# Optimization experiments

Hardware: AMD Instinct MI355X
Metric: run time of the kernel (lower is better)

Reference implementation:

```python
import jax, jax.numpy as jnp
import numpy as np

N_NODES = 20000
N_EDGES = 320000
D_IN = 256
DIMS = [512, 256, 128]
NEG_SLOPE = 0.2


def gatv2(x, src, dst, Wl, Wr, att, b, n):
    # GATv2Conv (heads=1, no self loops, no edge_attr)
    xl = x @ Wl                      # [N, D] source transform (lin_l)
    xr = x @ Wr                      # [N, D] target transform (lin_r)
    e = jax.nn.leaky_relu(xl[src] + xr[dst], NEG_SLOPE) @ att  # [E]
    # segment softmax over destination nodes
    m = jax.ops.segment_max(e, dst, num_segments=n)
    ex = jnp.exp(e - m[dst])
    s = jax.ops.segment_sum(ex, dst, num_segments=n)
    alpha = ex / (s[dst] + 1e-16)
    out = jax.ops.segment_sum(alpha[:, None] * xl[src], dst, num_segments=n)
    return out + b


def setup_inputs() -> dict:
    key = jax.random.key(0)
    ks = jax.random.split(key, 32)
    x = jax.random.normal(ks[0], (N_NODES, D_IN), dtype=jnp.float32)
    edge_index = jax.random.randint(ks[1], (2, N_EDGES), 0, N_NODES, dtype=jnp.int32)
    inp = {"x": x, "edge_index": edge_index}
    d_in = D_IN
    ki = 2
    for li, d_out in enumerate(DIMS, start=1):
        sc = 1.0 / np.sqrt(d_in)
        inp[f"Wl{li}"] = jax.random.normal(ks[ki + 0], (d_in, d_out), dtype=jnp.float32) * sc
        inp[f"Wr{li}"] = jax.random.normal(ks[ki + 1], (d_in, d_out), dtype=jnp.float32) * sc
        inp[f"att{li}"] = jax.random.normal(ks[ki + 2], (d_out,), dtype=jnp.float32) * (1.0 / np.sqrt(d_out))
        inp[f"bc{li}"] = jnp.zeros((d_out,), dtype=jnp.float32)
        inp[f"Ws{li}"] = jax.random.normal(ks[ki + 3], (d_in, d_out), dtype=jnp.float32) * sc
        inp[f"bs{li}"] = jnp.zeros((d_out,), dtype=jnp.float32)
        ki += 4
        d_in = d_out
    return inp


def reference(x, edge_index,
              Wl1, Wr1, att1, bc1, Ws1, bs1,
              Wl2, Wr2, att2, bc2, Ws2, bs2,
              Wl3, Wr3, att3, bc3, Ws3, bs3):
    src, dst = edge_index[0], edge_index[1]
    n = x.shape[0]
    h = gatv2(x, src, dst, Wl1, Wr1, att1, bc1, n) + (x @ Ws1 + bs1)
    h = jax.nn.relu(h)
    h = gatv2(h, src, dst, Wl2, Wr2, att2, bc2, n) + (h @ Ws2 + bs2)
    h = jax.nn.relu(h)
    h = gatv2(h, src, dst, Wl3, Wr3, att3, bc3, n) + (h @ Ws3 + bs3)
    return h
```

## Files before the change

kernel.cpp:

```cpp
#include <hip/hip_runtime.h>
#include <hip/hip_bf16.h>
#include <math.h>

#define N_NODES 20000
#define N_EDGES 320000
#define MAXDEG 64

typedef _Float16 f16x8 __attribute__((ext_vector_type(8)));
typedef _Float16 h2 __attribute__((ext_vector_type(2)));
typedef float f32x4 __attribute__((ext_vector_type(4)));

__device__ __forceinline__ unsigned short f2h_bits(float f) {
    _Float16 h = (_Float16)f;
    return __builtin_bit_cast(unsigned short, h);
}

typedef const unsigned int __attribute__((address_space(1)))* gas_ptr;
typedef unsigned int __attribute__((address_space(3)))* las_ptr;
__device__ __forceinline__ void gld16(const unsigned short* g, unsigned short* l) {
    __builtin_amdgcn_global_load_lds((gas_ptr)(const void*)g, (las_ptr)(void*)l, 16, 0, 0);
}

__global__ void scatter_kernel(const int* __restrict__ src, const int* __restrict__ dst,
                               int* __restrict__ cnt, int* __restrict__ csr_pad, int E) {
    int i = blockIdx.x * blockDim.x + threadIdx.x;
    if (i < E) {
        int d = dst[i];
        int pos = atomicAdd(&cnt[d], 1);
        if (pos < MAXDEG) csr_pad[(d << 6) + pos] = src[i];
    }
}

struct PrepJobs {
    const float* W[9];
    unsigned short* Wt[9];
    int K[9];
    int D[9];
    int tbeg[10];
    const float* x;
    unsigned short* xh;
    int nconv4;
    int nconvb;
    int* cnt;
};
__global__ __launch_bounds__(256) void prep_kernel(PrepJobs jb) {
    int bid = blockIdx.x;
    int ntile = jb.tbeg[9];
    if (bid < ntile) {
        __shared__ float ld[32][33];
        int job = 0;
        while (bid >= jb.tbeg[job + 1]) ++job;
        int tl = bid - jb.tbeg[job];
        int K = jb.K[job], D = jb.D[job];
        int TK = K >> 5;
        int td = tl / TK, tk = tl - td * TK;
        int k0 = tk << 5, d0 = td << 5;
        int t = threadIdx.x;
        int c = t & 31, r0 = (t >> 5) << 2;
        const float* Wp = jb.W[job];
#pragma unroll
        for (int jj = 0; jj < 4; ++jj)
            ld[r0 + jj][c] = Wp[(size_t)(k0 + r0 + jj) * D + d0 + c];
        __syncthreads();
        unsigned short* Wtp = jb.Wt[job];
#pragma unroll
        for (int jj = 0; jj < 4; ++jj) {
            int dr = r0 + jj;
            Wtp[(size_t)(d0 + dr) * K + k0 + c] = f2h_bits(ld[c][dr]);
        }
    } else if (bid < ntile + jb.nconvb) {
        int cidx = (bid - ntile) * 256 + (int)threadIdx.x;
        if (cidx < jb.nconv4) {
            int base = cidx * 4;
            float4 v = *(const float4*)(jb.x + base);
            uint2 pk;
            pk.x = (unsigned int)f2h_bits(v.x) | ((unsigned int)f2h_bits(v.y) << 16);
            pk.y = (unsigned int)f2h_bits(v.z) | ((unsigned int)f2h_bits(v.w) << 16);
            *(uint2*)(jb.xh + base) = pk;
        }
    } else {
        int i = (bid - ntile - jb.nconvb) * 256 + (int)threadIdx.x;
        if (i < N_NODES) jb.cnt[i] = 0;
    }
}

template <int SEED_F32>
__global__ __launch_bounds__(256) void gemm3_kernel(
        const unsigned short* __restrict__ A,
        const unsigned short* __restrict__ Bt,
        unsigned short* __restrict__ xlh,
        unsigned short* __restrict__ xrh,
        unsigned short* __restrict__ seedh,
        float* __restrict__ seedf,
        const float* __restrict__ b1,
        const float* __restrict__ b2,
        int M, int K, int D) {
    __shared__ __align__(16) unsigned short Asl[128 * 64];
    __shared__ __align__(16) unsigned short Bsl[128 * 64];

    int NC = (3 * D) >> 7;
    int MT = (M + 127) >> 7;
    int g = blockIdx.x;
    int xcd = g & 7, slot = g >> 3;
    int m_local = slot / NC, c = slot - m_local * NC;
    int mt = m_local * 8 + xcd;
    if (mt >= MT) return;

    int tid = threadIdx.x;
    int wave = tid >> 6, lane = tid & 63;
    int q = lane >> 4, t = lane & 15;
    int wm = (wave & 1) * 64, wn = (wave >> 1) * 64;
    int bm = mt << 7;
    int bn_all = c << 7;
    int seg = bn_all / D;
    int bn = bn_all - seg * D;

    f32x4 acc[4][4];
#pragma unroll
    for (int i = 0; i < 4; ++i)
#pragma unroll
        for (int j = 0; j < 4; ++j) acc[i][j] = (f32x4){0.f, 0.f, 0.f, 0.f};

    for (int k0 = 0; k0 < K; k0 += 64) {
#pragma unroll
        for (int rnd = 0; rnd < 4; ++rnd) {
            int ch = rnd * 256 + tid;
            int row = ch >> 3, part = ch & 7;
            int gr = bm + row; if (gr >= M) gr = M - 1;
            gld16(A + (size_t)gr * K + k0 + part * 8,
                  Asl + (rnd * 256 + wave * 64) * 8);
        }
#pragma unroll
        for (int rnd = 0; rnd < 4; ++rnd) {
            int ch = rnd * 256 + tid;
            int row = ch >> 3, part = ch & 7;
            gld16(Bt + (size_t)(bn_all + row) * K + k0 + part * 8,
                  Bsl + (rnd * 256 + wave * 64) * 8);
        }
        __syncthreads();

#pragma unroll
        for (int kk = 0; kk < 2; ++kk) {
            f16x8 an[4], am[4];
#pragma unroll
            for (int jn = 0; jn < 4; ++jn)
                an[jn] = *(const f16x8*)(Bsl + (wn + jn * 16 + t) * 64 + kk * 32 + q * 8);
#pragma unroll
            for (int im = 0; im < 4; ++im)
                am[im] = *(const f16x8*)(Asl + (wm + im * 16 + t) * 64 + kk * 32 + q * 8);
#pragma unroll
            for (int jn = 0; jn < 4; ++jn)
#pragma unroll
                for (int im = 0; im < 4; ++im)
                    acc[jn][im] = __builtin_amdgcn_mfma_f32_16x16x32_f16(an[jn], am[im], acc[jn][im], 0, 0, 0);
        }
        __syncthreads();
    }

#pragma unroll
    for (int jn = 0; jn < 4; ++jn) {
        int n0 = bn + wn + jn * 16 + q * 4;
        float bx = 0.f, by = 0.f, bz = 0.f, bw = 0.f;
        if (seg == 2) {
            float4 bb1 = *(const float4*)(b1 + n0);
            float4 bb2 = *(const float4*)(b2 + n0);
            bx = bb1.x + bb2.x; by = bb1.y + bb2.y;
            bz = bb1.z + bb2.z; bw = bb1.w + bb2.w;
        }
#pragma unroll
        for (int im = 0; im < 4; ++im) {
            int m = bm + wm + im * 16 + t;
            if (m < M) {
                float v0 = acc[jn][im][0] + bx;
                float v1 = acc[jn][im][1] + by;
                float v2 = acc[jn][im][2] + bz;
                float v3 = acc[jn][im][3] + bw;
                size_t idx = (size_t)m * D + n0;
                if (seg == 2 && SEED_F32) {
                    *(float4*)(seedf + idx) = make_float4(v0, v1, v2, v3);
                } else {
                    uint2 pk;
                    pk.x = (unsigned int)f2h_bits(v0) | ((unsigned int)f2h_bits(v1) << 16);
                    pk.y = (unsigned int)f2h_bits(v2) | ((unsigned int)f2h_bits(v3) << 16);
                    unsigned short* dstp = (seg == 0) ? xlh : (seg == 1) ? xrh : seedh;
                    *(uint2*)(dstp + idx) = pk;
                }
            }
        }
    }
}

template <int D, int SEED_H, int WRITE_H, int RELU>
__global__ __launch_bounds__(128) void fused_agg_kernel(
        const unsigned short* __restrict__ xl,
        const unsigned short* __restrict__ xr,
        const float* __restrict__ att,
        const int* __restrict__ cnt,
        const int* __restrict__ csr_pad,
        const unsigned short* __restrict__ seedh,
        const float* __restrict__ seedf,
        float* __restrict__ outf,
        unsigned short* __restrict__ outh) {
    constexpr int VPL = D / 64;
    constexpr int HP = VPL / 2;
    typedef _Float16 hvec __attribute__((ext_vector_type(VPL)));

    int wave = threadIdx.x >> 6, lane = threadIdx.x & 63;
    int n = blockIdx.x * 2 + wave;
    if (n >= N_NODES) return;
    int cn = cnt[n]; if (cn > MAXDEG) cn = MAXDEG;
    int beg = n << 6;
    int end = beg + cn;

    h2 xr_h[HP], att_h[HP];
    hvec xrv = *(const hvec*)(xr + (size_t)n * D + lane * VPL);
#pragma unroll
    for (int pp = 0; pp < HP; ++pp) {
        xr_h[pp] = (h2){xrv[2 * pp], xrv[2 * pp + 1]};
        att_h[pp] = (h2){(_Float16)att[lane * VPL + 2 * pp],
                         (_Float16)att[lane * VPL + 2 * pp + 1]};
    }

    float acc[VPL];
#pragma unroll
    for (int v = 0; v < VPL; ++v) acc[v] = 0.f;
    float m = -INFINITY, s = 0.f;

    const _Float16 c02 = (_Float16)0.2f;
    int lb0 = lane & 1;
    int lb1 = lane & 2;

    int nfull = cn >> 2;
    int j = beg;
    int i0 = 0, i1 = 0, i2 = 0, i3 = 0;
    if (nfull > 0) {
        i0 = csr_pad[beg]; i1 = csr_pad[beg + 1];
        i2 = csr_pad[beg + 2]; i3 = csr_pad[beg + 3];
    }
    for (int b = 0; b < nfull; ++b) {
        int s0 = i0, s1 = i1, s2 = i2, s3 = i3;
        int jn4 = j + 4;
        if (b + 1 < nfull) {
            i0 = csr_pad[jn4]; i1 = csr_pad[jn4 + 1];
            i2 = csr_pad[jn4 + 2]; i3 = csr_pad[jn4 + 3];
        }
        hvec x0 = *(const hvec*)(xl + (size_t)s0 * D + lane * VPL);
        hvec x1 = *(const hvec*)(xl + (size_t)s1 * D + lane * VPL);
        hvec x2 = *(const hvec*)(xl + (size_t)s2 * D + lane * VPL);
        hvec x3 = *(const hvec*)(xl + (size_t)s3 * D + lane * VPL);
        float p0 = 0.f, p1 = 0.f, p2 = 0.f, p3 = 0.f;
#pragma unroll
        for (int pp = 0; pp < HP; ++pp) {
            h2 a0 = (h2){x0[2 * pp], x0[2 * pp + 1]};
            h2 a1 = (h2){x1[2 * pp], x1[2 * pp + 1]};
            h2 a2 = (h2){x2[2 * pp], x2[2 * pp + 1]};
            h2 a3 = (h2){x3[2 * pp], x3[2 * pp + 1]};
            h2 z0 = a0 + xr_h[pp];
            h2 z1 = a1 + xr_h[pp];
            h2 z2 = a2 + xr_h[pp];
            h2 z3 = a3 + xr_h[pp];
            h2 l0 = __builtin_elementwise_max(z0, z0 * c02);
            h2 l1 = __builtin_elementwise_max(z1, z1 * c02);
            h2 l2 = __builtin_elementwise_max(z2, z2 * c02);
            h2 l3 = __builtin_elementwise_max(z3, z3 * c02);
#if __has_builtin(__builtin_amdgcn_fdot2)
            p0 = __builtin_amdgcn_fdot2(l0, att_h[pp], p0, false);
            p1 = __builtin_amdgcn_fdot2(l1, att_h[pp], p1, false);
            p2 = __builtin_amdgcn_fdot2(l2, att_h[pp], p2, false);
            p3 = __builtin_amdgcn_fdot2(l3, att_h[pp], p3, false);
#else
            p0 += (float)l0.x * (float)att_h[pp].x + (float)l0.y * (float)att_h[pp].y;
            p1 += (float)l1.x * (float)att_h[pp].x + (float)l1.y * (float)att_h[pp].y;
            p2 += (float)l2.x * (float)att_h[pp].x + (float)l2.y * (float)att_h[pp].y;
            p3 += (float)l3.x * (float)att_h[pp].x + (float)l3.y * (float)att_h[pp].y;
#endif
        }
        float k0 = lb0 ? p1 : p0, sn0 = lb0 ? p0 : p1;
        float k1 = lb0 ? p3 : p2, sn1 = lb0 ? p2 : p3;
        k0 += __shfl_xor(sn0, 1, 64);
        k1 += __shfl_xor(sn1, 1, 64);
        float k = lb1 ? k1 : k0, sn = lb1 ? k0 : k1;
        k += __shfl_xor(sn, 2, 64);
        k += __shfl_xor(k, 4, 64);
        k += __shfl_xor(k, 8, 64);
        k += __shfl_xor(k, 16, 64);
        k += __shfl_xor(k, 32, 64);
        float q0 = __shfl(k, 0, 64);
        float q1 = __shfl(k, 1, 64);
        float q2 = __shfl(k, 2, 64);
        float q3 = __shfl(k, 3, 64);

        float mn = fmaxf(m, fmaxf(fmaxf(q0, q1), fmaxf(q2, q3)));
        float sc = __expf(m - mn);
        float e0 = __expf(q0 - mn);
        float e1 = __expf(q1 - mn);
        float e2 = __expf(q2 - mn);
        float e3 = __expf(q3 - mn);
        s = s * sc + e0 + e1 + e2 + e3;
#pragma unroll
        for (int v = 0; v < VPL; ++v)
            acc[v] = acc[v] * sc + e0 * (float)x0[v] + e1 * (float)x1[v]
                                 + e2 * (float)x2[v] + e3 * (float)x3[v];
        m = mn;
        j = jn4;
    }
    for (; j < end; ++j) {
        int s0 = csr_pad[j];
        hvec x0 = *(const hvec*)(xl + (size_t)s0 * D + lane * VPL);
        float p0 = 0.f;
#pragma unroll
        for (int pp = 0; pp < HP; ++pp) {
            h2 a0 = (h2){x0[2 * pp], x0[2 * pp + 1]};
            h2 z0 = a0 + xr_h[pp];
            h2 l0 = __builtin_elementwise_max(z0, z0 * c02);
#if __has_builtin(__builtin_amdgcn_fdot2)
            p0 = __builtin_amdgcn_fdot2(l0, att_h[pp], p0, false);
#else
            p0 += (float)l0.x * (float)att_h[pp].x + (float)l0.y * (float)att_h[pp].y;
#endif
        }
#pragma unroll
        for (int o = 32; o > 0; o >>= 1) p0 += __shfl_xor(p0, o, 64);
        float mn = fmaxf(m, p0);
        float sc = __expf(m - mn);
        float e0 = __expf(p0 - mn);
        s = s * sc + e0;
#pragma unroll
        for (int v = 0; v < VPL; ++v) acc[v] = acc[v] * sc + e0 * (float)x0[v];
        m = mn;
    }

    float sinv = 1.0f / (s + 1e-16f);
    size_t base = (size_t)n * D + lane * VPL;
    float sd[VPL];
    if (SEED_H) {
        hvec sv = *(const hvec*)(seedh + base);
#pragma unroll
        for (int v = 0; v < VPL; ++v) sd[v] = (float)sv[v];
    } else {
#pragma unroll
        for (int v = 0; v < VPL; ++v) sd[v] = seedf[base + v];
    }
#pragma unroll
    for (int v = 0; v < VPL; ++v) {
        float val = sd[v] + acc[v] * sinv;
        if (RELU) val = fmaxf(val, 0.f);
        if (WRITE_H) outh[base + v] = f2h_bits(val);
        else         outf[base + v] = val;
    }
}

static void run_layer(const unsigned short* hact, int K, int D,
                      const unsigned short* Wcat,
                      const float* att, const float* bc, const float* bs,
                      unsigned short* xlh, unsigned short* xrh,
                      unsigned short* seedh, float* seedf,
                      const int* cnt, const int* csr_pad,
                      float* outf, unsigned short* outh, int final_layer,
                      hipStream_t stream) {
    int NC = 3 * D / 128;
    int MT = (N_NODES + 127) / 128;
    int nblk = 8 * ((MT + 7) / 8) * NC;
    if (final_layer)
        hipLaunchKernelGGL((gemm3_kernel<1>), dim3(nblk), dim3(256), 0, stream, hact, Wcat,
                           xlh, xrh, (unsigned short*)nullptr, seedf, bs, bc, N_NODES, K, D);
    else
        hipLaunchKernelGGL((gemm3_kernel<0>), dim3(nblk), dim3(256), 0, stream, hact, Wcat,
                           xlh, xrh, seedh, (float*)nullptr, bs, bc, N_NODES, K, D);

    dim3 agrid((N_NODES + 1) / 2);
    if (D == 512) {
        hipLaunchKernelGGL((fused_agg_kernel<512, 1, 1, 1>), agrid, dim3(128), 0, stream,
                           xlh, xrh, att, cnt, csr_pad, seedh, (const float*)nullptr,
                           (float*)nullptr, outh);
    } else if (D == 256) {
        hipLaunchKernelGGL((fused_agg_kernel<256, 1, 1, 1>), agrid, dim3(128), 0, stream,
                           xlh, xrh, att, cnt, csr_pad, seedh, (const float*)nullptr,
                           (float*)nullptr, outh);
    } else {
        hipLaunchKernelGGL((fused_agg_kernel<128, 0, 0, 0>), agrid, dim3(128), 0, stream,
                           xlh, xrh, att, cnt, csr_pad, (const unsigned short*)nullptr, seedf,
                           outf, (unsigned short*)nullptr);
    }
}

extern "C" void kernel_launch(void* const* d_in, const int* in_sizes, int n_in,
                              void* d_out, int out_size, void* d_ws, size_t ws_size,
                              hipStream_t stream) {
    const float* x = (const float*)d_in[0];
    const int* ei = (const int*)d_in[1];
    const int* src = ei;
    const int* dst = ei + N_EDGES;

    const float* Wl1 = (const float*)d_in[2];
    const float* Wr1 = (const float*)d_in[3];
    const float* att1 = (const float*)d_in[4];
    const float* bc1 = (const float*)d_in[5];
    const float* Ws1 = (const float*)d_in[6];
    const float* bs1 = (const float*)d_in[7];
    const float* Wl2 = (const float*)d_in[8];
    const float* Wr2 = (const float*)d_in[9];
    const float* att2 = (const float*)d_in[10];
    const float* bc2 = (const float*)d_in[11];
    const float* Ws2 = (const float*)d_in[12];
    const float* bs2 = (const float*)d_in[13];
    const float* Wl3 = (const float*)d_in[14];
    const float* Wr3 = (const float*)d_in[15];
    const float* att3 = (const float*)d_in[16];
    const float* bc3 = (const float*)d_in[17];
    const float* Ws3 = (const float*)d_in[18];
    const float* bs3 = (const float*)d_in[19];

    const size_t NF = (size_t)N_NODES * 512;
    const size_t NH = (size_t)N_NODES * 256;
    unsigned short* xlh   = (unsigned short*)d_ws;
    unsigned short* xrh   = xlh + NF;
    unsigned short* seedh = xrh + NF;
    unsigned short* xhf   = seedh + NF;
    unsigned short* h1h   = xhf + NH;
    unsigned short* h2h   = h1h + NF;
    unsigned short* Wcat1 = h2h + NH;
    unsigned short* Wcat2 = Wcat1 + 3 * 512 * 256;
    unsigned short* Wcat3 = Wcat2 + 3 * 256 * 512;
    int* cnt     = (int*)(Wcat3 + 3 * 128 * 256);
    int* csr_pad = cnt + N_NODES;
    size_t needed = (size_t)((char*)(csr_pad + (size_t)N_NODES * MAXDEG) - (char*)d_ws);
    if (ws_size < needed) return;

    {
        PrepJobs jb;
        const float* Ws_[9]  = {Wl1, Wr1, Ws1, Wl2, Wr2, Ws2, Wl3, Wr3, Ws3};
        unsigned short* Wt_[9] = {Wcat1, Wcat1 + 512 * 256, Wcat1 + 2 * 512 * 256,
                                  Wcat2, Wcat2 + 256 * 512, Wcat2 + 2 * 256 * 512,
                                  Wcat3, Wcat3 + 128 * 256, Wcat3 + 2 * 128 * 256};
        int K_[9] = {256, 256, 256, 512, 512, 512, 256, 256, 256};
        int D_[9] = {512, 512, 512, 256, 256, 256, 128, 128, 128};
        int o = 0;
        for (int i = 0; i < 9; ++i) {
            jb.W[i] = Ws_[i]; jb.Wt[i] = Wt_[i]; jb.K[i] = K_[i]; jb.D[i] = D_[i];
            jb.tbeg[i] = o; o += (K_[i] >> 5) * (D_[i] >> 5);
        }
        jb.tbeg[9] = o;
        jb.x = x;
        jb.xh = xhf;
        jb.nconv4 = N_NODES * 256 / 4;
        jb.nconvb = (jb.nconv4 + 255) / 256;
        jb.cnt = cnt;
        int nzerob = (N_NODES + 255) / 256;
        hipLaunchKernelGGL(prep_kernel, dim3(o + jb.nconvb + nzerob), dim3(256), 0, stream, jb);
    }
    hipLaunchKernelGGL(scatter_kernel, dim3((N_EDGES + 255) / 256), dim3(256), 0, stream,
                       src, dst, cnt, csr_pad, N_EDGES);

    run_layer(xhf, 256, 512, Wcat1, att1, bc1, bs1,
              xlh, xrh, seedh, (float*)nullptr, cnt, csr_pad,
              (float*)nullptr, h1h, 0, stream);
    run_layer(h1h, 512, 256, Wcat2, att2, bc2, bs2,
              xlh, xrh, seedh, (float*)nullptr, cnt, csr_pad,
              (float*)nullptr, h2h, 0, stream);
    run_layer(h2h, 256, 128, Wcat3, att3, bc3, bs3,
              xlh, xrh, (unsigned short*)nullptr, (float*)d_out, cnt, csr_pad,
              (float*)d_out, (unsigned short*)nullptr, 1, stream);
}
```

Baseline: 322.8 us.

## Fold CSR scatter into first GEMM launch and make aggregation grid-stride

The edge scatter that builds the padded CSR now runs as extra blocks appended to the layer-1 GEMM launch instead of as its own kernel. This removes one launch and lets the atomic scatter overlap with GEMM tiles. The aggregation kernel switches from one block per node pair to a fixed 2048-block grid-stride loop, so the attention vector is loaded once per wave rather than once per node. The trade-off is fewer resident waves for hiding gather latency and a possible load imbalance at the tail.

```diff
diff --git a/kernel.cpp b/kernel.cpp
--- a/kernel.cpp
+++ b/kernel.cpp
@@ -19,16 +19,6 @@
 typedef unsigned int __attribute__((address_space(3)))* las_ptr;
 __device__ __forceinline__ void gld16(const unsigned short* g, unsigned short* l) {
     __builtin_amdgcn_global_load_lds((gas_ptr)(const void*)g, (las_ptr)(void*)l, 16, 0, 0);
-}
-
-__global__ void scatter_kernel(const int* __restrict__ src, const int* __restrict__ dst,
-                               int* __restrict__ cnt, int* __restrict__ csr_pad, int E) {
-    int i = blockIdx.x * blockDim.x + threadIdx.x;
-    if (i < E) {
-        int d = dst[i];
-        int pos = atomicAdd(&cnt[d], 1);
-        if (pos < MAXDEG) csr_pad[(d << 6) + pos] = src[i];
-    }
 }
 
 struct PrepJobs {
@@ -94,13 +84,28 @@
         float* __restrict__ seedf,
         const float* __restrict__ b1,
         const float* __restrict__ b2,
-        int M, int K, int D) {
+        int M, int K, int D,
+        const int* __restrict__ sc_src,
+        const int* __restrict__ sc_dst,
+        int* __restrict__ sc_cnt,
+        int* __restrict__ sc_csr,
+        int scatterE, int gemm_nblk) {
     __shared__ __align__(16) unsigned short Asl[128 * 64];
     __shared__ __align__(16) unsigned short Bsl[128 * 64];
 
+    int g = blockIdx.x;
+    if (g >= gemm_nblk) {
+        int i = (g - gemm_nblk) * 256 + (int)threadIdx.x;
+        if (i < scatterE) {
+            int d = sc_dst[i];
+            int pos = atomicAdd(&sc_cnt[d], 1);
+            if (pos < MAXDEG) sc_csr[(d << 6) + pos] = sc_src[i];
+        }
+        return;
+    }
+
     int NC = (3 * D) >> 7;
     int MT = (M + 127) >> 7;
-    int g = blockIdx.x;
     int xcd = g & 7, slot = g >> 3;
     int m_local = slot / NC, c = slot - m_local * NC;
     int mt = m_local * 8 + xcd;
@@ -190,6 +195,8 @@
     }
 }
 
+#define AGG_BLOCKS 2048
+
 template <int D, int SEED_H, int WRITE_H, int RELU>
 __global__ __launch_bounds__(128) void fused_agg_kernel(
         const unsigned short* __restrict__ xl,
@@ -206,147 +213,151 @@
     typedef _Float16 hvec __attribute__((ext_vector_type(VPL)));
 
     int wave = threadIdx.x >> 6, lane = threadIdx.x & 63;
-    int n = blockIdx.x * 2 + wave;
-    if (n >= N_NODES) return;
-    int cn = cnt[n]; if (cn > MAXDEG) cn = MAXDEG;
-    int beg = n << 6;
-    int end = beg + cn;
-
-    h2 xr_h[HP], att_h[HP];
-    hvec xrv = *(const hvec*)(xr + (size_t)n * D + lane * VPL);
-#pragma unroll
-    for (int pp = 0; pp < HP; ++pp) {
-        xr_h[pp] = (h2){xrv[2 * pp], xrv[2 * pp + 1]};
-        att_h[pp] = (h2){(_Float16)att[lane * VPL + 2 * pp],
-                         (_Float16)att[lane * VPL + 2 * pp + 1]};
-    }
-
-    float acc[VPL];
-#pragma unroll
-    for (int v = 0; v < VPL; ++v) acc[v] = 0.f;
-    float m = -INFINITY, s = 0.f;
-
     const _Float16 c02 = (_Float16)0.2f;
     int lb0 = lane & 1;
     int lb1 = lane & 2;
 
-    int nfull = cn >> 2;
-    int j = beg;
-    int i0 = 0, i1 = 0, i2 = 0, i3 = 0;
-    if (nfull > 0) {
-        i0 = csr_pad[beg]; i1 = csr_pad[beg + 1];
-        i2 = csr_pad[beg + 2]; i3 = csr_pad[beg + 3];
-    }
-    for (int b = 0; b < nfull; ++b) {
-        int s0 = i0, s1 = i1, s2 = i2, s3 = i3;
-        int jn4 = j + 4;
-        if (b + 1 < nfull) {
-            i0 = csr_pad[jn4]; i1 = csr_pad[jn4 + 1];
-            i2 = csr_pad[jn4 + 2]; i3 = csr_pad[jn4 + 3];
-        }
-        hvec x0 = *(const hvec*)(xl + (size_t)s0 * D + lane * VPL);
-        hvec x1 = *(const hvec*)(xl + (size_t)s1 * D + lane * VPL);
-        hvec x2 = *(const hvec*)(xl + (size_t)s2 * D + lane * VPL);
-        hvec x3 = *(const hvec*)(xl + (size_t)s3 * D + lane * VPL);
-        float p0 = 0.f, p1 = 0.f, p2 = 0.f, p3 = 0.f;
-#pragma unroll
-        for (int pp = 0; pp < HP; ++pp) {
-            h2 a0 = (h2){x0[2 * pp], x0[2 * pp + 1]};
-            h2 a1 = (h2){x1[2 * pp], x1[2 * pp + 1]};
-            h2 a2 = (h2){x2[2 * pp], x2[2 * pp + 1]};
-            h2 a3 = (h2){x3[2 * pp], x3[2 * pp + 1]};
-            h2 z0 = a0 + xr_h[pp];
-            h2 z1 = a1 + xr_h[pp];
-            h2 z2 = a2 + xr_h[pp];
-            h2 z3 = a3 + xr_h[pp];
-            h2 l0 = __builtin_elementwise_max(z0, z0 * c02);
-            h2 l1 = __builtin_elementwise_max(z1, z1 * c02);
-            h2 l2 = __builtin_elementwise_max(z2, z2 * c02);
-            h2 l3 = __builtin_elementwise_max(z3, z3 * c02);
+    h2 att_h[HP];
+#pragma unroll
+    for (int pp = 0; pp < HP; ++pp)
+        att_h[pp] = (h2){(_Float16)att[lane * VPL + 2 * pp],
+                         (_Float16)att[lane * VPL + 2 * pp + 1]};
+
+    int nstride = (int)gridDim.x * 2;
+    for (int n = blockIdx.x * 2 + wave; n < N_NODES; n += nstride) {
+        int cn = cnt[n]; if (cn > MAXDEG) cn = MAXDEG;
+        int beg = n << 6;
+        int end = beg + cn;
+
+        h2 xr_h[HP];
+        hvec xrv = *(const hvec*)(xr + (size_t)n * D + lane * VPL);
+#pragma unroll
+        for (int pp = 0; pp < HP; ++pp)
+            xr_h[pp] = (h2){xrv[2 * pp], xrv[2 * pp + 1]};
+
+        float acc[VPL];
+#pragma unroll
+        for (int v = 0; v < VPL; ++v) acc[v] = 0.f;
+        float m = -INFINITY, s = 0.f;
+
+        int nfull = cn >> 2;
+        int j = beg;
+        int i0 = 0, i1 = 0, i2 = 0, i3 = 0;
+        if (nfull > 0) {
+            i0 = csr_pad[beg]; i1 = csr_pad[beg + 1];
+            i2 = csr_pad[beg + 2]; i3 = csr_pad[beg + 3];
+        }
+        for (int b = 0; b < nfull; ++b) {
+            int s0 = i0, s1 = i1, s2 = i2, s3 = i3;
+            int jn4 = j + 4;
+            if (b + 1 < nfull) {
+                i0 = csr_pad[jn4]; i1 = csr_pad[jn4 + 1];
+                i2 = csr_pad[jn4 + 2]; i3 = csr_pad[jn4 + 3];
+            }
+            hvec x0 = *(const hvec*)(xl + (size_t)s0 * D + lane * VPL);
+            hvec x1 = *(const hvec*)(xl + (size_t)s1 * D + lane * VPL);
+            hvec x2 = *(const hvec*)(xl + (size_t)s2 * D + lane * VPL);
+            hvec x3 = *(const hvec*)(xl + (size_t)s3 * D + lane * VPL);
+            float p0 = 0.f, p1 = 0.f, p2 = 0.f, p3 = 0.f;
+#pragma unroll
+            for (int pp = 0; pp < HP; ++pp) {
+                h2 a0 = (h2){x0[2 * pp], x0[2 * pp + 1]};
+                h2 a1 = (h2){x1[2 * pp], x1[2 * pp + 1]};
+                h2 a2 = (h2){x2[2 * pp], x2[2 * pp + 1]};
+                h2 a3 = (h2){x3[2 * pp], x3[2 * pp + 1]};
+                h2 z0 = a0 + xr_h[pp];
+                h2 z1 = a1 + xr_h[pp];
+                h2 z2 = a2 + xr_h[pp];
+                h2 z3 = a3 + xr_h[pp];
+                h2 l0 = __builtin_elementwise_max(z0, z0 * c02);
+                h2 l1 = __builtin_elementwise_max(z1, z1 * c02);
+                h2 l2 = __builtin_elementwise_max(z2, z2 * c02);
+                h2 l3 = __builtin_elementwise_max(z3, z3 * c02);
 #if __has_builtin(__builtin_amdgcn_fdot2)
-            p0 = __builtin_amdgcn_fdot2(l0, att_h[pp], p0, false);
-            p1 = __builtin_amdgcn_fdot2(l1, att_h[pp], p1, false);
-            p2 = __builtin_amdgcn_fdot2(l2, att_h[pp], p2, false);
-            p3 = __builtin_amdgcn_fdot2(l3, att_h[pp], p3, false);
+                p0 = __builtin_amdgcn_fdot2(l0, att_h[pp], p0, false);
+                p1 = __builtin_amdgcn_fdot2(l1, att_h[pp], p1, false);
+                p2 = __builtin_amdgcn_fdot2(l2, att_h[pp], p2, false);
+                p3 = __builtin_amdgcn_fdot2(l3, att_h[pp], p3, false);
 #else
-            p0 += (float)l0.x * (float)att_h[pp].x + (float)l0.y * (float)att_h[pp].y;
-            p1 += (float)l1.x * (float)att_h[pp].x + (float)l1.y * (float)att_h[pp].y;
-            p2 += (float)l2.x * (float)att_h[pp].x + (float)l2.y * (float)att_h[pp].y;
-            p3 += (float)l3.x * (float)att_h[pp].x + (float)l3.y * (float)att_h[pp].y;
+                p0 += (float)l0.x * (float)att_h[pp].x + (float)l0.y * (float)att_h[pp].y;
+                p1 += (float)l1.x * (float)att_h[pp].x + (float)l1.y * (float)att_h[pp].y;
+                p2 += (float)l2.x * (float)att_h[pp].x + (float)l2.y * (float)att_h[pp].y;
+                p3 += (float)l3.x * (float)att_h[pp].x + (float)l3.y * (float)att_h[pp].y;
 #endif
-        }
-        float k0 = lb0 ? p1 : p0, sn0 = lb0 ? p0 : p1;
-        float k1 = lb0 ? p3 : p2, sn1 = lb0 ? p2 : p3;
-        k0 += __shfl_xor(sn0, 1, 64);
-        k1 += __shfl_xor(sn1, 1, 64);
-        float k = lb1 ? k1 : k0, sn = lb1 ? k0 : k1;
-        k += __shfl_xor(sn, 2, 64);
-        k += __shfl_xor(k, 4, 64);
-        k += __shfl_xor(k, 8, 64);
-        k += __shfl_xor(k, 16, 64);
-        k += __shfl_xor(k, 32, 64);
-        float q0 = __shfl(k, 0, 64);
-        float q1 = __shfl(k, 1, 64);
-        float q2 = __shfl(k, 2, 64);
-        float q3 = __shfl(k, 3, 64);
-
-        float mn = fmaxf(m, fmaxf(fmaxf(q0, q1), fmaxf(q2, q3)));
-        float sc = __expf(m - mn);
-        float e0 = __expf(q0 - mn);
-        float e1 = __expf(q1 - mn);
-        float e2 = __expf(q2 - mn);
-        float e3 = __expf(q3 - mn);
-        s = s * sc + e0 + e1 + e2 + e3;
-#pragma unroll
-        for (int v = 0; v < VPL; ++v)
-            acc[v] = acc[v] * sc + e0 * (float)x0[v] + e1 * (float)x1[v]
-                                 + e2 * (float)x2[v] + e3 * (float)x3[v];
-        m = mn;
-        j = jn4;
-    }
-    for (; j < end; ++j) {
-        int s0 = csr_pad[j];
-        hvec x0 = *(const hvec*)(xl + (size_t)s0 * D + lane * VPL);
-        float p0 = 0.f;
-#pragma unroll
-        for (int pp = 0; pp < HP; ++pp) {
-            h2 a0 = (h2){x0[2 * pp], x0[2 * pp + 1]};
-            h2 z0 = a0 + xr_h[pp];
-            h2 l0 = __builtin_elementwise_max(z0, z0 * c02);
+            }
+            float k0 = lb0 ? p1 : p0, sn0 = lb0 ? p0 : p1;
+            float k1 = lb0 ? p3 : p2, sn1 = lb0 ? p2 : p3;
+            k0 += __shfl_xor(sn0, 1, 64);
+            k1 += __shfl_xor(sn1, 1, 64);
+            float k = lb1 ? k1 : k0, sn = lb1 ? k0 : k1;
+            k += __shfl_xor(sn, 2, 64);
+            k += __shfl_xor(k, 4, 64);
+            k += __shfl_xor(k, 8, 64);
+            k += __shfl_xor(k, 16, 64);
+            k += __shfl_xor(k, 32, 64);
+            float q0 = __shfl(k, 0, 64);
+            float q1 = __shfl(k, 1, 64);
+            float q2 = __shfl(k, 2, 64);
+            float q3 = __shfl(k, 3, 64);
+
+            float mn = fmaxf(m, fmaxf(fmaxf(q0, q1), fmaxf(q2, q3)));
+            float sc = __expf(m - mn);
+            float e0 = __expf(q0 - mn);
+            float e1 = __expf(q1 - mn);
+            float e2 = __expf(q2 - mn);
+            float e3 = __expf(q3 - mn);
+            s = s * sc + e0 + e1 + e2 + e3;
+#pragma unroll
+            for (int v = 0; v < VPL; ++v)
+                acc[v] = acc[v] * sc + e0 * (float)x0[v] + e1 * (float)x1[v]
+                                     + e2 * (float)x2[v] + e3 * (float)x3[v];
+            m = mn;
+            j = jn4;
+        }
+        for (; j < end; ++j) {
+            int s0 = csr_pad[j];
+            hvec x0 = *(const hvec*)(xl + (size_t)s0 * D + lane * VPL);
+            float p0 = 0.f;
+#pragma unroll
+            for (int pp = 0; pp < HP; ++pp) {
+                h2 a0 = (h2){x0[2 * pp], x0[2 * pp + 1]};
+                h2 z0 = a0 + xr_h[pp];
+                h2 l0 = __builtin_elementwise_max(z0, z0 * c02);
 #if __has_builtin(__builtin_amdgcn_fdot2)
-            p0 = __builtin_amdgcn_fdot2(l0, att_h[pp], p0, false);
+                p0 = __builtin_amdgcn_fdot2(l0, att_h[pp], p0, false);
 #else
-            p0 += (float)l0.x * (float)att_h[pp].x + (float)l0.y * (float)att_h[pp].y;
+                p0 += (float)l0.x * (float)att_h[pp].x + (float)l0.y * (float)att_h[pp].y;
 #endif
-        }
-#pragma unroll
-        for (int o = 32; o > 0; o >>= 1) p0 += __shfl_xor(p0, o, 64);
-        float mn = fmaxf(m, p0);
-        float sc = __expf(m - mn);
-        float e0 = __expf(p0 - mn);
-        s = s * sc + e0;
-#pragma unroll
-        for (int v = 0; v < VPL; ++v) acc[v] = acc[v] * sc + e0 * (float)x0[v];
-        m = mn;
-    }
-
-    float sinv = 1.0f / (s + 1e-16f);
-    size_t base = (size_t)n * D + lane * VPL;
-    float sd[VPL];
-    if (SEED_H) {
-        hvec sv = *(const hvec*)(seedh + base);
-#pragma unroll
-        for (int v = 0; v < VPL; ++v) sd[v] = (float)sv[v];
-    } else {
-#pragma unroll
-        for (int v = 0; v < VPL; ++v) sd[v] = seedf[base + v];
-    }
-#pragma unroll
-    for (int v = 0; v < VPL; ++v) {
-        float val = sd[v] + acc[v] * sinv;
-        if (RELU) val = fmaxf(val, 0.f);
-        if (WRITE_H) outh[base + v] = f2h_bits(val);
-        else         outf[base + v] = val;
+            }
+#pragma unroll
+            for (int o = 32; o > 0; o >>= 1) p0 += __shfl_xor(p0, o, 64);
+            float mn = fmaxf(m, p0);
+            float sc = __expf(m - mn);
+            float e0 = __expf(p0 - mn);
+            s = s * sc + e0;
+#pragma unroll
+            for (int v = 0; v < VPL; ++v) acc[v] = acc[v] * sc + e0 * (float)x0[v];
+            m = mn;
+        }
+
+        float sinv = 1.0f / (s + 1e-16f);
+        size_t base = (size_t)n * D + lane * VPL;
+        float sd[VPL];
+        if (SEED_H) {
+            hvec sv = *(const hvec*)(seedh + base);
+#pragma unroll
+            for (int v = 0; v < VPL; ++v) sd[v] = (float)sv[v];
+        } else {
+#pragma unroll
+            for (int v = 0; v < VPL; ++v) sd[v] = seedf[base + v];
+        }
+#pragma unroll
+        for (int v = 0; v < VPL; ++v) {
+            float val = sd[v] + acc[v] * sinv;
+            if (RELU) val = fmaxf(val, 0.f);
+            if (WRITE_H) outh[base + v] = f2h_bits(val);
+            else         outf[base + v] = val;
+        }
     }
 }
 
@@ -357,18 +368,23 @@
                       unsigned short* seedh, float* seedf,
                       const int* cnt, const int* csr_pad,
                       float* outf, unsigned short* outh, int final_layer,
+                      const int* sc_src, const int* sc_dst,
+                      int* sc_cnt, int* sc_csr, int scatterE,
                       hipStream_t stream) {
     int NC = 3 * D / 128;
     int MT = (N_NODES + 127) / 128;
     int nblk = 8 * ((MT + 7) / 8) * NC;
+    int sblk = (scatterE > 0) ? (scatterE + 255) / 256 : 0;
     if (final_layer)
-        hipLaunchKernelGGL((gemm3_kernel<1>), dim3(nblk), dim3(256), 0, stream, hact, Wcat,
-                           xlh, xrh, (unsigned short*)nullptr, seedf, bs, bc, N_NODES, K, D);
+        hipLaunchKernelGGL((gemm3_kernel<1>), dim3(nblk + sblk), dim3(256), 0, stream,
+                           hact, Wcat, xlh, xrh, (unsigned short*)nullptr, seedf, bs, bc,
+                           N_NODES, K, D, sc_src, sc_dst, sc_cnt, sc_csr, scatterE, nblk);
     else
-        hipLaunchKernelGGL((gemm3_kernel<0>), dim3(nblk), dim3(256), 0, stream, hact, Wcat,
-                           xlh, xrh, seedh, (float*)nullptr, bs, bc, N_NODES, K, D);
-
-    dim3 agrid((N_NODES + 1) / 2);
+        hipLaunchKernelGGL((gemm3_kernel<0>), dim3(nblk + sblk), dim3(256), 0, stream,
+                           hact, Wcat, xlh, xrh, seedh, (float*)nullptr, bs, bc,
+                           N_NODES, K, D, sc_src, sc_dst, sc_cnt, sc_csr, scatterE, nblk);
+
+    dim3 agrid(AGG_BLOCKS);
     if (D == 512) {
         hipLaunchKernelGGL((fused_agg_kernel<512, 1, 1, 1>), agrid, dim3(128), 0, stream,
                            xlh, xrh, att, cnt, csr_pad, seedh, (const float*)nullptr,
@@ -449,16 +465,17 @@
         int nzerob = (N_NODES + 255) / 256;
         hipLaunchKernelGGL(prep_kernel, dim3(o + jb.nconvb + nzerob), dim3(256), 0, stream, jb);
     }
-    hipLaunchKernelGGL(scatter_kernel, dim3((N_EDGES + 255) / 256), dim3(256), 0, stream,
-                       src, dst, cnt, csr_pad, N_EDGES);
 
     run_layer(xhf, 256, 512, Wcat1, att1, bc1, bs1,
               xlh, xrh, seedh, (float*)nullptr, cnt, csr_pad,
-              (float*)nullptr, h1h, 0, stream);
+              (float*)nullptr, h1h, 0,
+              src, dst, cnt, csr_pad, N_EDGES, stream);
     run_layer(h1h, 512, 256, Wcat2, att2, bc2, bs2,
               xlh, xrh, seedh, (float*)nullptr, cnt, csr_pad,
-              (float*)nullptr, h2h, 0, stream);
+              (float*)nullptr, h2h, 0,
+              (const int*)nullptr, (const int*)nullptr, (int*)nullptr, (int*)nullptr, 0, stream);
     run_layer(h2h, 256, 128, Wcat3, att3, bc3, bs3,
               xlh, xrh, (unsigned short*)nullptr, (float*)d_out, cnt, csr_pad,
-              (float*)d_out, (unsigned short*)nullptr, 1, stream);
-}
+              (float*)d_out, (unsigned short*)nullptr, 1,
+              (const int*)nullptr, (const int*)nullptr, (int*)nullptr, (int*)nullptr, 0, stream);
+}
```

After: 333.1 us. 3.2% more time.
